# Performance work log

Hardware: AMD Instinct MI355X
Metric: run time of the kernel (lower is better)

The kernel has to match this reference:

```python
import jax, jax.numpy as jnp
import numpy as np

N, K, D, H = 2048, 128, 768, 512


def setup_inputs() -> dict:
    key = jax.random.key(0)
    k1, k2, k3, k4, k5, k6 = jax.random.split(key, 6)
    image_feat = jax.random.normal(k1, (N, D), dtype=jnp.float32)
    text_feat = jax.random.normal(k2, (K, D), dtype=jnp.float32)
    # nn.Linear(2D, H): weight (H, 2D), bias (H); stored transposed for clean matmul
    W1 = jax.random.normal(k3, (2 * D, H), dtype=jnp.float32) * (1.0 / np.sqrt(2 * D))
    b1 = jax.random.normal(k4, (H,), dtype=jnp.float32) * 0.01
    # nn.Linear(H, 1)
    W2 = jax.random.normal(k5, (H, 1), dtype=jnp.float32) * (1.0 / np.sqrt(H))
    b2 = jax.random.normal(k6, (1,), dtype=jnp.float32) * 0.01
    return {"image_feat": image_feat, "text_feat": text_feat,
            "W1": W1, "b1": b1, "W2": W2, "b2": b2}


def reference(image_feat, text_feat, W1, b1, W2, b2):
    # concat([img, txt]) @ W1 == img @ W1[:D] + txt @ W1[D:]  (same math,
    # avoids materializing the (N,K,2D) concatenated tensor)
    img_proj = image_feat @ W1[:D]          # (N, H)
    txt_proj = text_feat @ W1[D:]           # (K, H)
    h = jax.nn.relu(img_proj[:, None, :] + txt_proj[None, :, :] + b1)  # (N, K, H)
    sim = (h @ W2).squeeze(-1) + b2[0]      # (N, K)
    return sim
```

## Files before the change

### kernel.cpp

```cpp
#include <hip/hip_runtime.h>
#include <hip/hip_bf16.h>

#define N_IMG 2048
#define K_TXT 128
#define D_IN  768
#define H_DIM 512
#define M_TOT (N_IMG + K_TXT)
#define NK    (N_IMG * K_TXT)

typedef __bf16 bf16x8 __attribute__((ext_vector_type(8)));
typedef float  f32x4  __attribute__((ext_vector_type(4)));

__global__ __launch_bounds__(256) void proj_kernel(
    const float* __restrict__ img, const float* __restrict__ txt,
    const float* __restrict__ W1, const float* __restrict__ b1,
    const float* __restrict__ W2, float* __restrict__ P,
    float* __restrict__ pw)
{
    __shared__ __align__(16) __bf16 As[32][72];
    __shared__ __align__(16) __bf16 Bs[64][72];

    const int tid = threadIdx.x;
    const int n0 = (blockIdx.x & 7) * 64;
    const int m0 = (blockIdx.x >> 3) * 32;
    const bool is_txt = (m0 >= N_IMG);
    const float* X  = is_txt ? (txt + (size_t)(m0 - N_IMG) * D_IN)
                             : (img + (size_t)m0 * D_IN);
    const float* Wb = W1 + (is_txt ? (size_t)D_IN * H_DIM : 0);

    const int wave = tid >> 6, lane = tid & 63;
    const int wm = (wave >> 1) * 16, wn = (wave & 1) * 32;
    const int quad = lane >> 4, lm = lane & 15;

    const int ar = tid >> 3, ak = (tid & 7) * 8;
    const int bn = tid & 63, bk = (tid >> 6) * 16;

    f32x4 acc[2] = {};
    f32x4 aR0, aR1;
    float bR[16];

    auto loadA = [&](int kc) {
        const float* ap = X + (size_t)ar * D_IN + kc + ak;
        aR0 = *(const f32x4*)(ap + 0);
        aR1 = *(const f32x4*)(ap + 4);
    };
    auto loadB = [&](int kc) {
        #pragma unroll
        for (int j = 0; j < 16; ++j)
            bR[j] = Wb[(size_t)(kc + bk + j) * H_DIM + n0 + bn];
    };

    union BPack { __bf16 h[8]; uint4 u; };

    loadA(0); loadB(0);

    for (int it = 0; it < 12; ++it) {
        BPack pa;
        #pragma unroll
        for (int j = 0; j < 4; ++j) { pa.h[j] = (__bf16)aR0[j]; pa.h[4+j] = (__bf16)aR1[j]; }
        *(uint4*)&As[ar][ak] = pa.u;
        BPack q0, q1;
        #pragma unroll
        for (int j = 0; j < 8; ++j) { q0.h[j] = (__bf16)bR[j]; q1.h[j] = (__bf16)bR[8+j]; }
        *(uint4*)&Bs[bn][bk]     = q0.u;
        *(uint4*)&Bs[bn][bk + 8] = q1.u;
        __syncthreads();

        if (it < 11) { loadA((it + 1) * 64); loadB((it + 1) * 64); }

        #pragma unroll
        for (int sub = 0; sub < 2; ++sub) {
            bf16x8 af  = *(bf16x8*)&As[wm + lm][sub * 32 + quad * 8];
            bf16x8 bf0 = *(bf16x8*)&Bs[wn +  0 + lm][sub * 32 + quad * 8];
            bf16x8 bf1 = *(bf16x8*)&Bs[wn + 16 + lm][sub * 32 + quad * 8];
            acc[0] = __builtin_amdgcn_mfma_f32_16x16x32_bf16(af, bf0, acc[0], 0, 0, 0);
            acc[1] = __builtin_amdgcn_mfma_f32_16x16x32_bf16(af, bf1, acc[1], 0, 0, 0);
        }
        __syncthreads();
    }

    float rv[4] = {0.f, 0.f, 0.f, 0.f};
    #pragma unroll
    for (int j = 0; j < 2; ++j) {
        const int gn = n0 + wn + j * 16 + lm;
        const float badd = is_txt ? b1[gn] : 0.0f;
        const float w2h = 0.5f * W2[gn];
        #pragma unroll
        for (int r = 0; r < 4; ++r) {
            const int gm = m0 + wm + quad * 4 + r;
            const float v = acc[j][r] + badd;
            P[(size_t)gm * H_DIM + gn] = v;
            rv[r] = fmaf(v, w2h, rv[r]);
        }
    }
    #pragma unroll
    for (int m = 1; m < 16; m <<= 1) {
        #pragma unroll
        for (int r = 0; r < 4; ++r) rv[r] += __shfl_xor(rv[r], m, 64);
    }
    if (lm == 0) {
        #pragma unroll
        for (int r = 0; r < 4; ++r)
            atomicAdd(&pw[m0 + wm + quad * 4 + r], rv[r]);
    }
}

__global__ __launch_bounds__(256) void sim_kernel(
    const float* __restrict__ P, const float* __restrict__ W2,
    float* __restrict__ P2)
{
    __shared__ __align__(16) float Bs[64][67];
    __shared__ __align__(16) float Ws[64];

    const int tid = threadIdx.x;
    const int n0 = blockIdx.x * 32;
    const int k0 = blockIdx.y * 64;
    const int hs = blockIdx.z;
    const int hc = hs * 64;

    #pragma unroll
    for (int i = 0; i < 4; ++i) {
        const int flat = tid + i * 256;
        const int row = flat >> 4, c4 = flat & 15;
        f32x4 v = *(const f32x4*)(P + (size_t)(N_IMG + k0 + row) * H_DIM + hc + c4 * 4);
        *(f32x4*)&Bs[row][c4 * 4] = v;
    }
    if (tid < 16) {
        f32x4 w = *(const f32x4*)(W2 + hc + tid * 4);
        w *= 0.5f;
        *(f32x4*)&Ws[tid * 4] = w;
    }
    __syncthreads();

    const int tx = tid & 15;
    const int ty = tid >> 4;
    const float* pA = P + (size_t)(n0 + ty * 2) * H_DIM + hc;

    f32x4 acc0 = {0.f, 0.f, 0.f, 0.f};
    f32x4 acc1 = {0.f, 0.f, 0.f, 0.f};

    #pragma unroll 4
    for (int h4 = 0; h4 < 16; ++h4) {
        f32x4 a0 = *(const f32x4*)(pA + h4 * 4);
        f32x4 a1 = *(const f32x4*)(pA + H_DIM + h4 * 4);
        f32x4 w  = *(f32x4*)&Ws[h4 * 4];
        f32x4 b[4];
        #pragma unroll
        for (int j = 0; j < 4; ++j) b[j] = *(f32x4*)&Bs[tx * 4 + j][h4 * 4];

        #pragma unroll
        for (int j = 0; j < 4; ++j) {
            #pragma unroll
            for (int hh = 0; hh < 4; ++hh) {
                const float t0 = a0[hh] + b[j][hh];
                acc0[j] = fmaf(fabsf(t0), w[hh], acc0[j]);
                const float t1 = a1[hh] + b[j][hh];
                acc1[j] = fmaf(fabsf(t1), w[hh], acc1[j]);
            }
        }
    }

    float* o = P2 + (size_t)hs * NK + (size_t)(n0 + ty * 2) * K_TXT + k0 + tx * 4;
    *(f32x4*)o = acc0;
    *(f32x4*)(o + K_TXT) = acc1;
}

__global__ __launch_bounds__(256) void reduce_kernel(
    const float* __restrict__ P2, const float* __restrict__ pw,
    const float* __restrict__ b2, float* __restrict__ out)
{
    const int idx = blockIdx.x * 256 + threadIdx.x;
    const int n  = idx >> 5;
    const int k4 = (idx & 31) * 4;
    const size_t base = (size_t)n * K_TXT + k4;

    f32x4 s = {0.f, 0.f, 0.f, 0.f};
    #pragma unroll
    for (int hs = 0; hs < 8; ++hs)
        s += *(const f32x4*)(P2 + (size_t)hs * NK + base);

    const float add = pw[n] + b2[0];
    f32x4 pk = *(const f32x4*)(pw + N_IMG + k4);
    s[0] += add + pk[0]; s[1] += add + pk[1];
    s[2] += add + pk[2]; s[3] += add + pk[3];
    *(f32x4*)(out + base) = s;
}

extern "C" void kernel_launch(void* const* d_in, const int* in_sizes, int n_in,
                              void* d_out, int out_size, void* d_ws, size_t ws_size,
                              hipStream_t stream) {
    const float* img = (const float*)d_in[0];
    const float* txt = (const float*)d_in[1];
    const float* W1  = (const float*)d_in[2];
    const float* b1  = (const float*)d_in[3];
    const float* W2  = (const float*)d_in[4];
    const float* b2  = (const float*)d_in[5];
    float* out = (float*)d_out;

    float* P  = (float*)d_ws;
    float* pw = P + (size_t)M_TOT * H_DIM;
    float* P2 = pw + M_TOT;

    hipMemsetAsync(pw, 0, M_TOT * sizeof(float), stream);

    proj_kernel  <<<dim3(544),                256, 0, stream>>>(img, txt, W1, b1, W2, P, pw);
    sim_kernel   <<<dim3(N_IMG / 32, K_TXT / 64, H_DIM / 64), 256, 0, stream>>>(P, W2, P2);
    reduce_kernel<<<dim3(NK / 4 / 256),       256, 0, stream>>>(P2, pw, b2, out);
}
```

Baseline: 101.7 us.

## Halve projection tile width and replace global atomics with per-tile partial sums

The projection GEMM now uses 32-wide column tiles, doubling the block count from 544 to 1088 so more of the GPU is busy. The per-row w2 partial sums are first reduced in shared memory and then written to a per-column-tile slice instead of going through global atomics. This removes the memset launch, and the reduce kernel sums the 16 slices itself. In exchange, each block does half the MFMA work per A-tile load, so the A operand is re-read from global memory twice as often, and the reduce kernel makes extra scattered reads.

```diff
diff --git a/kernel.cpp b/kernel.cpp
--- a/kernel.cpp
+++ b/kernel.cpp
@@ -7,6 +7,7 @@
 #define H_DIM 512
 #define M_TOT (N_IMG + K_TXT)
 #define NK    (N_IMG * K_TXT)
+#define NTILE 16
 
 typedef __bf16 bf16x8 __attribute__((ext_vector_type(8)));
 typedef float  f32x4  __attribute__((ext_vector_type(4)));
@@ -15,29 +16,30 @@
     const float* __restrict__ img, const float* __restrict__ txt,
     const float* __restrict__ W1, const float* __restrict__ b1,
     const float* __restrict__ W2, float* __restrict__ P,
-    float* __restrict__ pw)
+    float* __restrict__ pw2)
 {
     __shared__ __align__(16) __bf16 As[32][72];
-    __shared__ __align__(16) __bf16 Bs[64][72];
+    __shared__ __align__(16) __bf16 Bs[32][72];
+    __shared__ float lds_pw[32];
 
     const int tid = threadIdx.x;
-    const int n0 = (blockIdx.x & 7) * 64;
-    const int m0 = (blockIdx.x >> 3) * 32;
+    const int n0 = (blockIdx.x & (NTILE - 1)) * 32;
+    const int m0 = (blockIdx.x >> 4) * 32;
     const bool is_txt = (m0 >= N_IMG);
     const float* X  = is_txt ? (txt + (size_t)(m0 - N_IMG) * D_IN)
                              : (img + (size_t)m0 * D_IN);
     const float* Wb = W1 + (is_txt ? (size_t)D_IN * H_DIM : 0);
 
     const int wave = tid >> 6, lane = tid & 63;
-    const int wm = (wave >> 1) * 16, wn = (wave & 1) * 32;
+    const int wm = (wave >> 1) * 16, wn = (wave & 1) * 16;
     const int quad = lane >> 4, lm = lane & 15;
 
     const int ar = tid >> 3, ak = (tid & 7) * 8;
-    const int bn = tid & 63, bk = (tid >> 6) * 16;
-
-    f32x4 acc[2] = {};
+    const int bn = tid & 31, bk = (tid >> 5) * 8;
+
+    f32x4 acc = {0.f, 0.f, 0.f, 0.f};
     f32x4 aR0, aR1;
-    float bR[16];
+    float bR[8];
 
     auto loadA = [&](int kc) {
         const float* ap = X + (size_t)ar * D_IN + kc + ak;
@@ -46,7 +48,7 @@
     };
     auto loadB = [&](int kc) {
         #pragma unroll
-        for (int j = 0; j < 16; ++j)
+        for (int j = 0; j < 8; ++j)
             bR[j] = Wb[(size_t)(kc + bk + j) * H_DIM + n0 + bn];
     };
 
@@ -59,38 +61,34 @@
         #pragma unroll
         for (int j = 0; j < 4; ++j) { pa.h[j] = (__bf16)aR0[j]; pa.h[4+j] = (__bf16)aR1[j]; }
         *(uint4*)&As[ar][ak] = pa.u;
-        BPack q0, q1;
-        #pragma unroll
-        for (int j = 0; j < 8; ++j) { q0.h[j] = (__bf16)bR[j]; q1.h[j] = (__bf16)bR[8+j]; }
-        *(uint4*)&Bs[bn][bk]     = q0.u;
-        *(uint4*)&Bs[bn][bk + 8] = q1.u;
+        BPack q;
+        #pragma unroll
+        for (int j = 0; j < 8; ++j) q.h[j] = (__bf16)bR[j];
+        *(uint4*)&Bs[bn][bk] = q.u;
         __syncthreads();
 
         if (it < 11) { loadA((it + 1) * 64); loadB((it + 1) * 64); }
 
         #pragma unroll
         for (int sub = 0; sub < 2; ++sub) {
-            bf16x8 af  = *(bf16x8*)&As[wm + lm][sub * 32 + quad * 8];
-            bf16x8 bf0 = *(bf16x8*)&Bs[wn +  0 + lm][sub * 32 + quad * 8];
-            bf16x8 bf1 = *(bf16x8*)&Bs[wn + 16 + lm][sub * 32 + quad * 8];
-            acc[0] = __builtin_amdgcn_mfma_f32_16x16x32_bf16(af, bf0, acc[0], 0, 0, 0);
-            acc[1] = __builtin_amdgcn_mfma_f32_16x16x32_bf16(af, bf1, acc[1], 0, 0, 0);
+            bf16x8 af = *(bf16x8*)&As[wm + lm][sub * 32 + quad * 8];
+            bf16x8 bf = *(bf16x8*)&Bs[wn + lm][sub * 32 + quad * 8];
+            acc = __builtin_amdgcn_mfma_f32_16x16x32_bf16(af, bf, acc, 0, 0, 0);
         }
         __syncthreads();
     }
 
-    float rv[4] = {0.f, 0.f, 0.f, 0.f};
-    #pragma unroll
-    for (int j = 0; j < 2; ++j) {
-        const int gn = n0 + wn + j * 16 + lm;
+    float rv[4];
+    {
+        const int gn = n0 + wn + lm;
         const float badd = is_txt ? b1[gn] : 0.0f;
         const float w2h = 0.5f * W2[gn];
         #pragma unroll
         for (int r = 0; r < 4; ++r) {
             const int gm = m0 + wm + quad * 4 + r;
-            const float v = acc[j][r] + badd;
+            const float v = acc[r] + badd;
             P[(size_t)gm * H_DIM + gn] = v;
-            rv[r] = fmaf(v, w2h, rv[r]);
+            rv[r] = v * w2h;
         }
     }
     #pragma unroll
@@ -98,11 +96,16 @@
         #pragma unroll
         for (int r = 0; r < 4; ++r) rv[r] += __shfl_xor(rv[r], m, 64);
     }
+    if (tid < 32) lds_pw[tid] = 0.f;
+    __syncthreads();
     if (lm == 0) {
         #pragma unroll
         for (int r = 0; r < 4; ++r)
-            atomicAdd(&pw[m0 + wm + quad * 4 + r], rv[r]);
-    }
+            atomicAdd(&lds_pw[wm + quad * 4 + r], rv[r]);
+    }
+    __syncthreads();
+    if (tid < 32)
+        pw2[(size_t)(blockIdx.x & (NTILE - 1)) * M_TOT + m0 + tid] = lds_pw[tid];
 }
 
 __global__ __launch_bounds__(256) void sim_kernel(
@@ -166,7 +169,7 @@
 }
 
 __global__ __launch_bounds__(256) void reduce_kernel(
-    const float* __restrict__ P2, const float* __restrict__ pw,
+    const float* __restrict__ P2, const float* __restrict__ pw2,
     const float* __restrict__ b2, float* __restrict__ out)
 {
     const int idx = blockIdx.x * 256 + threadIdx.x;
@@ -179,8 +182,16 @@
     for (int hs = 0; hs < 8; ++hs)
         s += *(const f32x4*)(P2 + (size_t)hs * NK + base);
 
-    const float add = pw[n] + b2[0];
-    f32x4 pk = *(const f32x4*)(pw + N_IMG + k4);
+    float pn = 0.f;
+    f32x4 pk = {0.f, 0.f, 0.f, 0.f};
+    #pragma unroll
+    for (int sl = 0; sl < NTILE; ++sl) {
+        const float* pws = pw2 + (size_t)sl * M_TOT;
+        pn += pws[n];
+        pk += *(const f32x4*)(pws + N_IMG + k4);
+    }
+
+    const float add = pn + b2[0];
     s[0] += add + pk[0]; s[1] += add + pk[1];
     s[2] += add + pk[2]; s[3] += add + pk[3];
     *(f32x4*)(out + base) = s;
@@ -197,13 +208,11 @@
     const float* b2  = (const float*)d_in[5];
     float* out = (float*)d_out;
 
-    float* P  = (float*)d_ws;
-    float* pw = P + (size_t)M_TOT * H_DIM;
-    float* P2 = pw + M_TOT;
-
-    hipMemsetAsync(pw, 0, M_TOT * sizeof(float), stream);
-
-    proj_kernel  <<<dim3(544),                256, 0, stream>>>(img, txt, W1, b1, W2, P, pw);
+    float* P   = (float*)d_ws;
+    float* pw2 = P + (size_t)M_TOT * H_DIM;
+    float* P2  = pw2 + (size_t)NTILE * M_TOT;
+
+    proj_kernel  <<<dim3(68 * NTILE),           256, 0, stream>>>(img, txt, W1, b1, W2, P, pw2);
     sim_kernel   <<<dim3(N_IMG / 32, K_TXT / 64, H_DIM / 64), 256, 0, stream>>>(P, W2, P2);
-    reduce_kernel<<<dim3(NK / 4 / 256),       256, 0, stream>>>(P2, pw, b2, out);
-}
+    reduce_kernel<<<dim3(NK / 4 / 256),         256, 0, stream>>>(P2, pw2, b2, out);
+}
```

Result: no change. 100.6 us (-1.1%).
